# Performance work log

Hardware: AMD Instinct MI355X
Metric: run time of the kernel (lower is better)

## Reference

```python
import jax, jax.numpy as jnp
import numpy as np

B, CIN, COUT, H, W, K, PAD = 8, 64, 64, 128, 128, 3, 1
KK = K * K


def setup_inputs() -> dict:
    key = jax.random.key(0)
    k1, k2, k3, k4 = jax.random.split(key, 4)
    x = jax.random.normal(k1, (B, CIN, H, W), jnp.float32)
    # offset/mask conv: 3*K*K output channels (2*KK offsets + KK mask logits).
    # Original zero-inits these; we use small random weights so the irregular
    # gather path is actually exercised (zero offsets degenerate to plain conv).
    w_off = jax.random.normal(k2, (3 * KK, CIN, K, K), jnp.float32) * 0.01
    b_off = jax.random.normal(k3, (3 * KK,), jnp.float32) * 0.01
    w_dcn = jax.random.normal(k4, (COUT, CIN, K, K), jnp.float32) * (1.0 / np.sqrt(CIN * KK))
    return {"x": x, "w_off": w_off, "b_off": b_off, "w_dcn": w_dcn}


def _bilinear_gather(x, py, px):
    # x: [B,C,H,W]; py/px: [B,KK,H,W] float sample coordinates.
    # Zero padding: integer corners outside the image contribute 0 (torchvision semantics).
    Bn, C, Hn, Wn = x.shape
    y0 = jnp.floor(py).astype(jnp.int32)
    x0 = jnp.floor(px).astype(jnp.int32)
    y1, x1 = y0 + 1, x0 + 1
    wy1 = py - y0.astype(py.dtype)
    wy0 = 1.0 - wy1
    wx1 = px - x0.astype(px.dtype)
    wx0 = 1.0 - wx1
    xf = x.reshape(Bn, C, Hn * Wn)

    def g(iy, ix):
        valid = ((iy >= 0) & (iy < Hn) & (ix >= 0) & (ix < Wn)).astype(x.dtype)
        idx = (jnp.clip(iy, 0, Hn - 1) * Wn + jnp.clip(ix, 0, Wn - 1)).reshape(Bn, -1)
        v = jax.vmap(lambda xr, i: xr[:, i])(xf, idx).reshape(Bn, C, *iy.shape[1:])
        return v * valid[:, None]  # [B,C,KK,H,W]

    return ((wy0 * wx0)[:, None] * g(y0, x0) + (wy0 * wx1)[:, None] * g(y0, x1)
            + (wy1 * wx0)[:, None] * g(y1, x0) + (wy1 * wx1)[:, None] * g(y1, x1))


def reference(x, w_off, b_off, w_dcn):
    dn = ('NCHW', 'OIHW', 'NCHW')
    off = jax.lax.conv_general_dilated(x, w_off, (1, 1), [(PAD, PAD), (PAD, PAD)],
                                       dimension_numbers=dn) + b_off[None, :, None, None]
    o1, o2, m = off[:, :KK], off[:, KK:2 * KK], off[:, 2 * KK:]
    mask = jax.nn.sigmoid(m)                    # [B,KK,H,W]
    offset = jnp.concatenate([o1, o2], axis=1)  # [B,2KK,H,W], torch cat((o1,o2),dim=1)
    # torchvision interprets channel 2k as dy, 2k+1 as dx for kernel point k
    dy, dx = offset[:, 0::2], offset[:, 1::2]   # each [B,KK,H,W]
    ki = (jnp.arange(KK) // K - PAD).astype(x.dtype)
    kj = (jnp.arange(KK) % K - PAD).astype(x.dtype)
    py = jnp.arange(H, dtype=x.dtype)[None, None, :, None] + ki[None, :, None, None] + dy
    px = jnp.arange(W, dtype=x.dtype)[None, None, None, :] + kj[None, :, None, None] + dx
    val = _bilinear_gather(x, py, px) * mask[:, None]  # [B,C,KK,H,W]
    return jnp.einsum('bckhw,ock->bohw', val, w_dcn.reshape(COUT, CIN, KK))
```

## Files before the change

kernel.cpp:

```cpp
#include <hip/hip_runtime.h>

#define Bn 8
#define CINn 64
#define COUTn 64
#define Hn 128
#define Wn 128
#define KKn 9

typedef __attribute__((ext_vector_type(8))) short short8v;
typedef __attribute__((ext_vector_type(4))) float f32x4;

__device__ __forceinline__ unsigned short f2bf(float f) {
    unsigned u = __float_as_uint(f);
    unsigned r = (u + 0x7FFFu + ((u >> 16) & 1u)) >> 16;
    return (unsigned short)r;
}
__device__ __forceinline__ float bf2f(unsigned short u) {
    return __uint_as_float(((unsigned)u) << 16);
}

__launch_bounds__(256)
__global__ void xt_prep(const float* __restrict__ x, unsigned short* __restrict__ xt) {
    __shared__ unsigned short tile[128 * 68];
    const int blk = blockIdx.x;
    const int b = blk >> 7, y = blk & 127;
    const int t = threadIdx.x;
    const float* xb = x + (((long)b * CINn) << 14) + (y << 7);
#pragma unroll
    for (int i = 0; i < 32; ++i) {
        int e = i * 256 + t;
        int c = e >> 7, xx = e & 127;
        tile[xx * 68 + c] = f2bf(xb[((long)c << 14) + xx]);
    }
    __syncthreads();
    unsigned short* dst = xt + ((long)(b * 128 + y) << 13);
#pragma unroll
    for (int i = 0; i < 4; ++i) {
        int q = i * 256 + t;
        int xx = q >> 3, j = q & 7;
        const unsigned long long* src = (const unsigned long long*)&tile[xx * 68 + j * 8];
        unsigned long long v0 = src[0], v1 = src[1];
        unsigned long long* d = (unsigned long long*)&dst[q * 8];
        d[0] = v0; d[1] = v1;
    }
}

__global__ void wdcn_prep(const float* __restrict__ w_dcn, unsigned short* __restrict__ w2) {
    int i = blockIdx.x * 256 + threadIdx.x;
    if (i >= COUTn * CINn * KKn) return;
    int c = i & 63;
    int o = (i >> 6) & 63;
    int k = i >> 12;
    w2[i] = f2bf(w_dcn[(o * CINn + c) * KKn + k]);
}

__global__ void woffprep(const float* __restrict__ w_off, unsigned short* __restrict__ wofft) {
    int i = blockIdx.x * 256 + threadIdx.x;
    if (i >= 9 * 32 * 64) return;
    int c   = i & 63;
    int ch  = (i >> 6) & 31;
    int tap = i >> 11;
    wofft[i] = (ch < 27) ? f2bf(w_off[(ch * 64 + c) * 9 + tap]) : (unsigned short)0;
}

__launch_bounds__(256)
__global__ void offconv_direct(const unsigned short* __restrict__ xt,
                               const unsigned short* __restrict__ wofft,
                               const float* __restrict__ b_off,
                               unsigned short* __restrict__ offo) {
    int blk = blockIdx.x;
    blk = (blk & 7) * 128 + (blk >> 3);
    const int b = blk >> 7, h = blk & 127;
    const int t = threadIdx.x;
    const int lane = t & 63, wv = t >> 6;
    const int r16 = lane & 15, sub = lane >> 4;
    const unsigned short* xtb = xt + ((long)b << 20);

    f32x4 acc[2][2];
#pragma unroll
    for (int mt = 0; mt < 2; ++mt)
#pragma unroll
        for (int ntl = 0; ntl < 2; ++ntl) acc[mt][ntl] = (f32x4){0.f, 0.f, 0.f, 0.f};

    const short8v zf = {0, 0, 0, 0, 0, 0, 0, 0};

#pragma unroll
    for (int di = 0; di < 3; ++di) {
        const int y = h + di - 1;
        const bool yok = (y >= 0 && y < Hn);
#pragma unroll
        for (int dj = 0; dj < 3; ++dj) {
            const int tap = di * 3 + dj;
#pragma unroll
            for (int kk = 0; kk < 2; ++kk) {
                const int cc8 = (kk * 4 + sub) << 3;
                short8v a0 = *(const short8v*)(wofft + ((tap * 32 +      r16) << 6) + cc8);
                short8v a1 = *(const short8v*)(wofft + ((tap * 32 + 16 + r16) << 6) + cc8);
                short8v bfr[2];
#pragma unroll
                for (int ntl = 0; ntl < 2; ++ntl) {
                    int w = wv * 32 + ntl * 16 + r16 + dj - 1;
                    bool valid = yok && (w >= 0 && w < Wn);
                    int wc = valid ? w : 0;
                    int yc = yok ? y : 0;
                    short8v v = *(const short8v*)(xtb + (yc << 13) + (wc << 6) + cc8);
                    bfr[ntl] = valid ? v : zf;
                }
#pragma unroll
                for (int ntl = 0; ntl < 2; ++ntl) {
                    acc[0][ntl] = __builtin_amdgcn_mfma_f32_16x16x32_bf16(a0, bfr[ntl], acc[0][ntl], 0, 0, 0);
                    acc[1][ntl] = __builtin_amdgcn_mfma_f32_16x16x32_bf16(a1, bfr[ntl], acc[1][ntl], 0, 0, 0);
                }
            }
        }
    }

#pragma unroll
    for (int mt = 0; mt < 2; ++mt)
#pragma unroll
        for (int ntl = 0; ntl < 2; ++ntl) {
            int w = wv * 32 + ntl * 16 + r16;
#pragma unroll
            for (int r = 0; r < 4; ++r) {
                int ch = mt * 16 + sub * 4 + r;
                if (ch < 27)
                    offo[(((long)(b * 27 + ch)) << 14) + (h << 7) + w] = f2bf(acc[mt][ntl][r] + b_off[ch]);
            }
        }
}

__launch_bounds__(256)
__global__ void dcn_direct(const unsigned short* __restrict__ xt,
                           const unsigned short* __restrict__ offo,
                           const unsigned short* __restrict__ w2,
                           float* __restrict__ out) {
    int blk = blockIdx.x;
    blk = (blk & 7) * 128 + (blk >> 3);
    const int b = blk >> 7, h = blk & 127;
    const int t = threadIdx.x;
    const int lane = t & 63, wv = t >> 6;
    const int r16 = lane & 15, sub = lane >> 4;
    const unsigned short* xtb = xt + ((long)b << 20);
    const unsigned short* ob  = offo + (((long)b * 27) << 14) + (h << 7);

    f32x4 acc[4][2];
#pragma unroll
    for (int ot = 0; ot < 4; ++ot)
#pragma unroll
        for (int ptl = 0; ptl < 2; ++ptl)
            acc[ot][ptl] = (f32x4){0.f, 0.f, 0.f, 0.f};

    for (int k = 0; k < KKn; ++k) {
        const int ky = k / 3 - 1, kx = k % 3 - 1;
        int o00[2], o01[2], o10[2], o11[2];
        float q00[2], q01[2], q10[2], q11[2];
#pragma unroll
        for (int ptl = 0; ptl < 2; ++ptl) {
            int pos = wv * 32 + ptl * 16 + r16;
            float dy = bf2f(ob[((long)(2 * k) << 14) + pos]);
            float dx = bf2f(ob[((long)(2 * k + 1) << 14) + pos]);
            float m  = bf2f(ob[((long)(18 + k) << 14) + pos]);
            m = 1.f / (1.f + __expf(-m));
            float py = (float)(h + ky) + dy;
            float px = (float)(pos + kx) + dx;
            float fy = floorf(py), fx = floorf(px);
            int y0 = (int)fy, x0 = (int)fx;
            float wy1 = py - fy, wx1 = px - fx;
            float a0 = (y0 >= 0     && y0 < Hn)     ? (1.f - wy1) * m : 0.f;
            float a1 = (y0 + 1 >= 0 && y0 + 1 < Hn) ? wy1 * m         : 0.f;
            float b0 = (x0 >= 0     && x0 < Wn)     ? (1.f - wx1)     : 0.f;
            float b1 = (x0 + 1 >= 0 && x0 + 1 < Wn) ? wx1             : 0.f;
            q00[ptl] = a0 * b0; q01[ptl] = a0 * b1; q10[ptl] = a1 * b0; q11[ptl] = a1 * b1;
            int y0c = min(max(y0, 0), Hn - 1), y1c = min(max(y0 + 1, 0), Hn - 1);
            int x0c = min(max(x0, 0), Wn - 1), x1c = min(max(x0 + 1, 0), Wn - 1);
            o00[ptl] = (y0c << 13) + (x0c << 6); o01[ptl] = (y0c << 13) + (x1c << 6);
            o10[ptl] = (y1c << 13) + (x0c << 6); o11[ptl] = (y1c << 13) + (x1c << 6);
        }

#pragma unroll
        for (int kk = 0; kk < 2; ++kk) {
            const int cc8 = (kk * 4 + sub) << 3;
            short8v af[4];
#pragma unroll
            for (int ot = 0; ot < 4; ++ot)
                af[ot] = *(const short8v*)(w2 + (k << 12) + ((ot * 16 + r16) << 6) + cc8);
            short8v bfr[2];
#pragma unroll
            for (int ptl = 0; ptl < 2; ++ptl) {
                short8v c00 = *(const short8v*)(xtb + o00[ptl] + cc8);
                short8v c01 = *(const short8v*)(xtb + o01[ptl] + cc8);
                short8v c10 = *(const short8v*)(xtb + o10[ptl] + cc8);
                short8v c11 = *(const short8v*)(xtb + o11[ptl] + cc8);
                const unsigned* u00 = (const unsigned*)&c00;
                const unsigned* u01 = (const unsigned*)&c01;
                const unsigned* u10 = (const unsigned*)&c10;
                const unsigned* u11 = (const unsigned*)&c11;
                short8v bf;
                unsigned* ub = (unsigned*)&bf;
#pragma unroll
                for (int jj = 0; jj < 4; ++jj) {
                    float f00l = __uint_as_float(u00[jj] << 16), f00h = __uint_as_float(u00[jj] & 0xffff0000u);
                    float f01l = __uint_as_float(u01[jj] << 16), f01h = __uint_as_float(u01[jj] & 0xffff0000u);
                    float f10l = __uint_as_float(u10[jj] << 16), f10h = __uint_as_float(u10[jj] & 0xffff0000u);
                    float f11l = __uint_as_float(u11[jj] << 16), f11h = __uint_as_float(u11[jj] & 0xffff0000u);
                    float tl = q00[ptl] * f00l + q01[ptl] * f01l + q10[ptl] * f10l + q11[ptl] * f11l;
                    float th = q00[ptl] * f00h + q01[ptl] * f01h + q10[ptl] * f10h + q11[ptl] * f11h;
                    ub[jj] = (unsigned)f2bf(tl) | ((unsigned)f2bf(th) << 16);
                }
                bfr[ptl] = bf;
            }
#pragma unroll
            for (int ot = 0; ot < 4; ++ot)
#pragma unroll
                for (int ptl = 0; ptl < 2; ++ptl)
                    acc[ot][ptl] = __builtin_amdgcn_mfma_f32_16x16x32_bf16(af[ot], bfr[ptl], acc[ot][ptl], 0, 0, 0);
        }
    }

    const long obase = (((long)b * COUTn) << 14) + (h << 7);
#pragma unroll
    for (int ot = 0; ot < 4; ++ot)
#pragma unroll
        for (int ptl = 0; ptl < 2; ++ptl) {
#pragma unroll
            for (int r = 0; r < 4; ++r) {
                int o   = ot * 16 + sub * 4 + r;
                int pos = wv * 32 + ptl * 16 + r16;
                out[obase + ((long)o << 14) + pos] = acc[ot][ptl][r];
            }
        }
}

extern "C" void kernel_launch(void* const* d_in, const int* in_sizes, int n_in,
                              void* d_out, int out_size, void* d_ws, size_t ws_size,
                              hipStream_t stream) {
    const float* x     = (const float*)d_in[0];
    const float* w_off = (const float*)d_in[1];
    const float* b_off = (const float*)d_in[2];
    const float* w_dcn = (const float*)d_in[3];
    float* out = (float*)d_out;

    unsigned short* xt    = (unsigned short*)d_ws;
    unsigned short* w2    = (unsigned short*)((char*)d_ws + 16777216);
    unsigned short* wofft = (unsigned short*)((char*)d_ws + 16850944);
    unsigned short* offo  = (unsigned short*)((char*)d_ws + 16887808);

    xt_prep<<<Bn * Hn, 256, 0, stream>>>(x, xt);
    wdcn_prep<<<144, 256, 0, stream>>>(w_dcn, w2);
    woffprep<<<72, 256, 0, stream>>>(w_off, wofft);
    offconv_direct<<<Bn * Hn, 256, 0, stream>>>(xt, wofft, b_off, offo);
    dcn_direct<<<Bn * Hn, 256, 0, stream>>>(xt, offo, w2, out);
}
```

Measured before the change: 242.4 us.

## Split each row across two blocks and store offsets pixel-major

Both the offset conv and DCN kernels now launch twice as many blocks. Each block covers half an image row, so each wave handles 16 pixels instead of 32, which increases parallelism and lowers register pressure. The offset buffer layout changes from channel-major to pixel-major with 32 channels per pixel, so each DCN thread reads its dy/dx pair with one 32-bit load and its mask nearby. In exchange, the weight fragment loads are amortised over fewer MFMAs per block, and the offset-conv stores become strided.

After: 282.1 us. 16.4% more time.

```diff
diff --git a/kernel.cpp b/kernel.cpp
--- a/kernel.cpp
+++ b/kernel.cpp
@@ -69,25 +69,24 @@
                                const float* __restrict__ b_off,
                                unsigned short* __restrict__ offo) {
     int blk = blockIdx.x;
-    blk = (blk & 7) * 128 + (blk >> 3);
-    const int b = blk >> 7, h = blk & 127;
+    blk = (blk & 7) * 256 + (blk >> 3);
+    const int b = blk >> 8, h = (blk >> 1) & 127, ph = blk & 1;
     const int t = threadIdx.x;
     const int lane = t & 63, wv = t >> 6;
     const int r16 = lane & 15, sub = lane >> 4;
+    const int wbase = ph * 64 + wv * 16;
     const unsigned short* xtb = xt + ((long)b << 20);
 
-    f32x4 acc[2][2];
-#pragma unroll
-    for (int mt = 0; mt < 2; ++mt)
-#pragma unroll
-        for (int ntl = 0; ntl < 2; ++ntl) acc[mt][ntl] = (f32x4){0.f, 0.f, 0.f, 0.f};
-
+    f32x4 acc[2];
+    acc[0] = (f32x4){0.f, 0.f, 0.f, 0.f};
+    acc[1] = (f32x4){0.f, 0.f, 0.f, 0.f};
     const short8v zf = {0, 0, 0, 0, 0, 0, 0, 0};
 
 #pragma unroll
     for (int di = 0; di < 3; ++di) {
         const int y = h + di - 1;
         const bool yok = (y >= 0 && y < Hn);
+        const int yc = yok ? y : 0;
 #pragma unroll
         for (int dj = 0; dj < 3; ++dj) {
             const int tap = di * 3 + dj;
@@ -96,37 +95,27 @@
                 const int cc8 = (kk * 4 + sub) << 3;
                 short8v a0 = *(const short8v*)(wofft + ((tap * 32 +      r16) << 6) + cc8);
                 short8v a1 = *(const short8v*)(wofft + ((tap * 32 + 16 + r16) << 6) + cc8);
-                short8v bfr[2];
-#pragma unroll
-                for (int ntl = 0; ntl < 2; ++ntl) {
-                    int w = wv * 32 + ntl * 16 + r16 + dj - 1;
-                    bool valid = yok && (w >= 0 && w < Wn);
-                    int wc = valid ? w : 0;
-                    int yc = yok ? y : 0;
-                    short8v v = *(const short8v*)(xtb + (yc << 13) + (wc << 6) + cc8);
-                    bfr[ntl] = valid ? v : zf;
-                }
-#pragma unroll
-                for (int ntl = 0; ntl < 2; ++ntl) {
-                    acc[0][ntl] = __builtin_amdgcn_mfma_f32_16x16x32_bf16(a0, bfr[ntl], acc[0][ntl], 0, 0, 0);
-                    acc[1][ntl] = __builtin_amdgcn_mfma_f32_16x16x32_bf16(a1, bfr[ntl], acc[1][ntl], 0, 0, 0);
-                }
+                int w = wbase + r16 + dj - 1;
+                bool valid = yok && (w >= 0 && w < Wn);
+                int wc = valid ? w : 0;
+                short8v v = *(const short8v*)(xtb + (yc << 13) + (wc << 6) + cc8);
+                short8v bfr = valid ? v : zf;
+                acc[0] = __builtin_amdgcn_mfma_f32_16x16x32_bf16(a0, bfr, acc[0], 0, 0, 0);
+                acc[1] = __builtin_amdgcn_mfma_f32_16x16x32_bf16(a1, bfr, acc[1], 0, 0, 0);
             }
         }
     }
 
-#pragma unroll
-    for (int mt = 0; mt < 2; ++mt)
-#pragma unroll
-        for (int ntl = 0; ntl < 2; ++ntl) {
-            int w = wv * 32 + ntl * 16 + r16;
-#pragma unroll
-            for (int r = 0; r < 4; ++r) {
-                int ch = mt * 16 + sub * 4 + r;
-                if (ch < 27)
-                    offo[(((long)(b * 27 + ch)) << 14) + (h << 7) + w] = f2bf(acc[mt][ntl][r] + b_off[ch]);
-            }
-        }
+    unsigned short* po = offo + ((((long)b << 7) + h) << 12) + ((wbase + r16) << 5);
+#pragma unroll
+    for (int mt = 0; mt < 2; ++mt) {
+#pragma unroll
+        for (int r = 0; r < 4; ++r) {
+            int ch = mt * 16 + sub * 4 + r;
+            if (ch < 27)
+                po[ch] = f2bf(acc[mt][r] + b_off[ch]);
+        }
+    }
 }
 
 __launch_bounds__(256)
@@ -135,47 +124,40 @@
                            const unsigned short* __restrict__ w2,
                            float* __restrict__ out) {
     int blk = blockIdx.x;
-    blk = (blk & 7) * 128 + (blk >> 3);
-    const int b = blk >> 7, h = blk & 127;
+    blk = (blk & 7) * 256 + (blk >> 3);
+    const int b = blk >> 8, h = (blk >> 1) & 127, ph = blk & 1;
     const int t = threadIdx.x;
     const int lane = t & 63, wv = t >> 6;
     const int r16 = lane & 15, sub = lane >> 4;
+    const int pos = ph * 64 + wv * 16 + r16;
     const unsigned short* xtb = xt + ((long)b << 20);
-    const unsigned short* ob  = offo + (((long)b * 27) << 14) + (h << 7);
-
-    f32x4 acc[4][2];
-#pragma unroll
-    for (int ot = 0; ot < 4; ++ot)
-#pragma unroll
-        for (int ptl = 0; ptl < 2; ++ptl)
-            acc[ot][ptl] = (f32x4){0.f, 0.f, 0.f, 0.f};
+    const unsigned short* pix = offo + ((((long)b << 7) + h) << 12) + (pos << 5);
+
+    f32x4 acc[4];
+#pragma unroll
+    for (int ot = 0; ot < 4; ++ot) acc[ot] = (f32x4){0.f, 0.f, 0.f, 0.f};
 
     for (int k = 0; k < KKn; ++k) {
         const int ky = k / 3 - 1, kx = k % 3 - 1;
-        int o00[2], o01[2], o10[2], o11[2];
-        float q00[2], q01[2], q10[2], q11[2];
-#pragma unroll
-        for (int ptl = 0; ptl < 2; ++ptl) {
-            int pos = wv * 32 + ptl * 16 + r16;
-            float dy = bf2f(ob[((long)(2 * k) << 14) + pos]);
-            float dx = bf2f(ob[((long)(2 * k + 1) << 14) + pos]);
-            float m  = bf2f(ob[((long)(18 + k) << 14) + pos]);
-            m = 1.f / (1.f + __expf(-m));
-            float py = (float)(h + ky) + dy;
-            float px = (float)(pos + kx) + dx;
-            float fy = floorf(py), fx = floorf(px);
-            int y0 = (int)fy, x0 = (int)fx;
-            float wy1 = py - fy, wx1 = px - fx;
-            float a0 = (y0 >= 0     && y0 < Hn)     ? (1.f - wy1) * m : 0.f;
-            float a1 = (y0 + 1 >= 0 && y0 + 1 < Hn) ? wy1 * m         : 0.f;
-            float b0 = (x0 >= 0     && x0 < Wn)     ? (1.f - wx1)     : 0.f;
-            float b1 = (x0 + 1 >= 0 && x0 + 1 < Wn) ? wx1             : 0.f;
-            q00[ptl] = a0 * b0; q01[ptl] = a0 * b1; q10[ptl] = a1 * b0; q11[ptl] = a1 * b1;
-            int y0c = min(max(y0, 0), Hn - 1), y1c = min(max(y0 + 1, 0), Hn - 1);
-            int x0c = min(max(x0, 0), Wn - 1), x1c = min(max(x0 + 1, 0), Wn - 1);
-            o00[ptl] = (y0c << 13) + (x0c << 6); o01[ptl] = (y0c << 13) + (x1c << 6);
-            o10[ptl] = (y1c << 13) + (x0c << 6); o11[ptl] = (y1c << 13) + (x1c << 6);
-        }
+        unsigned dydx = *(const unsigned*)(pix + 2 * k);
+        float dy = bf2f((unsigned short)(dydx & 0xffffu));
+        float dx = bf2f((unsigned short)(dydx >> 16));
+        float m  = bf2f(pix[18 + k]);
+        m = 1.f / (1.f + __expf(-m));
+        float py = (float)(h + ky) + dy;
+        float px = (float)(pos + kx) + dx;
+        float fy = floorf(py), fx = floorf(px);
+        int y0 = (int)fy, x0 = (int)fx;
+        float wy1 = py - fy, wx1 = px - fx;
+        float a0 = (y0 >= 0     && y0 < Hn)     ? (1.f - wy1) * m : 0.f;
+        float a1 = (y0 + 1 >= 0 && y0 + 1 < Hn) ? wy1 * m         : 0.f;
+        float b0 = (x0 >= 0     && x0 < Wn)     ? (1.f - wx1)     : 0.f;
+        float b1 = (x0 + 1 >= 0 && x0 + 1 < Wn) ? wx1             : 0.f;
+        float q00 = a0 * b0, q01 = a0 * b1, q10 = a1 * b0, q11 = a1 * b1;
+        int y0c = min(max(y0, 0), Hn - 1), y1c = min(max(y0 + 1, 0), Hn - 1);
+        int x0c = min(max(x0, 0), Wn - 1), x1c = min(max(x0 + 1, 0), Wn - 1);
+        int o00 = (y0c << 13) + (x0c << 6), o01 = (y0c << 13) + (x1c << 6);
+        int o10 = (y1c << 13) + (x0c << 6), o11 = (y1c << 13) + (x1c << 6);
 
 #pragma unroll
         for (int kk = 0; kk < 2; ++kk) {
@@ -184,51 +166,41 @@
 #pragma unroll
             for (int ot = 0; ot < 4; ++ot)
                 af[ot] = *(const short8v*)(w2 + (k << 12) + ((ot * 16 + r16) << 6) + cc8);
-            short8v bfr[2];
-#pragma unroll
-            for (int ptl = 0; ptl < 2; ++ptl) {
-                short8v c00 = *(const short8v*)(xtb + o00[ptl] + cc8);
-                short8v c01 = *(const short8v*)(xtb + o01[ptl] + cc8);
-                short8v c10 = *(const short8v*)(xtb + o10[ptl] + cc8);
-                short8v c11 = *(const short8v*)(xtb + o11[ptl] + cc8);
-                const unsigned* u00 = (const unsigned*)&c00;
-                const unsigned* u01 = (const unsigned*)&c01;
-                const unsigned* u10 = (const unsigned*)&c10;
-                const unsigned* u11 = (const unsigned*)&c11;
-                short8v bf;
-                unsigned* ub = (unsigned*)&bf;
-#pragma unroll
-                for (int jj = 0; jj < 4; ++jj) {
-                    float f00l = __uint_as_float(u00[jj] << 16), f00h = __uint_as_float(u00[jj] & 0xffff0000u);
-                    float f01l = __uint_as_float(u01[jj] << 16), f01h = __uint_as_float(u01[jj] & 0xffff0000u);
-                    float f10l = __uint_as_float(u10[jj] << 16), f10h = __uint_as_float(u10[jj] & 0xffff0000u);
-                    float f11l = __uint_as_float(u11[jj] << 16), f11h = __uint_as_float(u11[jj] & 0xffff0000u);
-                    float tl = q00[ptl] * f00l + q01[ptl] * f01l + q10[ptl] * f10l + q11[ptl] * f11l;
-                    float th = q00[ptl] * f00h + q01[ptl] * f01h + q10[ptl] * f10h + q11[ptl] * f11h;
-                    ub[jj] = (unsigned)f2bf(tl) | ((unsigned)f2bf(th) << 16);
-                }
-                bfr[ptl] = bf;
+            short8v c00 = *(const short8v*)(xtb + o00 + cc8);
+            short8v c01 = *(const short8v*)(xtb + o01 + cc8);
+            short8v c10 = *(const short8v*)(xtb + o10 + cc8);
+            short8v c11 = *(const short8v*)(xtb + o11 + cc8);
+            const unsigned* u00 = (const unsigned*)&c00;
+            const unsigned* u01 = (const unsigned*)&c01;
+            const unsigned* u10 = (const unsigned*)&c10;
+            const unsigned* u11 = (const unsigned*)&c11;
+            short8v bfv;
+            unsigned* ub = (unsigned*)&bfv;
+#pragma unroll
+            for (int jj = 0; jj < 4; ++jj) {
+                float f00l = __uint_as_float(u00[jj] << 16), f00h = __uint_as_float(u00[jj] & 0xffff0000u);
+                float f01l = __uint_as_float(u01[jj] << 16), f01h = __uint_as_float(u01[jj] & 0xffff0000u);
+                float f10l = __uint_as_float(u10[jj] << 16), f10h = __uint_as_float(u10[jj] & 0xffff0000u);
+                float f11l = __uint_as_float(u11[jj] << 16), f11h = __uint_as_float(u11[jj] & 0xffff0000u);
+                float tl = q00 * f00l + q01 * f01l + q10 * f10l + q11 * f11l;
+                float th = q00 * f00h + q01 * f01h + q10 * f10h + q11 * f11h;
+                ub[jj] = (unsigned)f2bf(tl) | ((unsigned)f2bf(th) << 16);
             }
 #pragma unroll
             for (int ot = 0; ot < 4; ++ot)
-#pragma unroll
-                for (int ptl = 0; ptl < 2; ++ptl)
-                    acc[ot][ptl] = __builtin_amdgcn_mfma_f32_16x16x32_bf16(af[ot], bfr[ptl], acc[ot][ptl], 0, 0, 0);
+                acc[ot] = __builtin_amdgcn_mfma_f32_16x16x32_bf16(af[ot], bfv, acc[ot], 0, 0, 0);
         }
     }
 
     const long obase = (((long)b * COUTn) << 14) + (h << 7);
 #pragma unroll
-    for (int ot = 0; ot < 4; ++ot)
-#pragma unroll
-        for (int ptl = 0; ptl < 2; ++ptl) {
-#pragma unroll
-            for (int r = 0; r < 4; ++r) {
-                int o   = ot * 16 + sub * 4 + r;
-                int pos = wv * 32 + ptl * 16 + r16;
-                out[obase + ((long)o << 14) + pos] = acc[ot][ptl][r];
-            }
-        }
+    for (int ot = 0; ot < 4; ++ot) {
+#pragma unroll
+        for (int r = 0; r < 4; ++r) {
+            int o = ot * 16 + sub * 4 + r;
+            out[obase + ((long)o << 14) + pos] = acc[ot][r];
+        }
+    }
 }
 
 extern "C" void kernel_launch(void* const* d_in, const int* in_sizes, int n_in,
@@ -248,6 +220,6 @@
     xt_prep<<<Bn * Hn, 256, 0, stream>>>(x, xt);
     wdcn_prep<<<144, 256, 0, stream>>>(w_dcn, w2);
     woffprep<<<72, 256, 0, stream>>>(w_off, wofft);
-    offconv_direct<<<Bn * Hn, 256, 0, stream>>>(xt, wofft, b_off, offo);
-    dcn_direct<<<Bn * Hn, 256, 0, stream>>>(xt, offo, w2, out);
-}
+    offconv_direct<<<2 * Bn * Hn, 256, 0, stream>>>(xt, wofft, b_off, offo);
+    dcn_direct<<<2 * Bn * Hn, 256, 0, stream>>>(xt, offo, w2, out);
+}
```
